# Kernel optimization log

Measured on AMD Instinct MI355X. Metric: run time of the kernel, lower is better.

## Reference

```python
import jax, jax.numpy as jnp
import numpy as np

N_NODES = 100000
N_EDGES = 1600000
HIDDEN = 128
NUM_RBF = 50
NTYPES = 95
CUTOFF = 5.0


def setup_inputs() -> dict:
    key = jax.random.key(0)
    ks = jax.random.split(key, 10)
    z = jax.random.randint(ks[0], (N_NODES,), 0, NTYPES)
    node_feat = jax.random.normal(ks[1], (N_NODES, HIDDEN), dtype=jnp.float32)
    edge_index = jax.random.randint(ks[2], (2, N_EDGES), 0, N_NODES)
    # distances uniform in [0, 6) so some edges fall beyond the 5.0 cutoff
    edge_weight = jax.random.uniform(ks[3], (N_EDGES,), dtype=jnp.float32) * 6.0
    edge_attr = jax.random.normal(ks[4], (N_EDGES, NUM_RBF), dtype=jnp.float32)
    # learned parameters
    emb = jax.random.normal(ks[5], (NTYPES, HIDDEN), dtype=jnp.float32)
    dp_w = jax.random.normal(ks[6], (HIDDEN, NUM_RBF), dtype=jnp.float32) * (1.0 / np.sqrt(NUM_RBF))
    dp_b = jnp.zeros((HIDDEN,), dtype=jnp.float32)
    comb_w = jax.random.normal(ks[7], (HIDDEN, 2 * HIDDEN), dtype=jnp.float32) * (1.0 / np.sqrt(2 * HIDDEN))
    comb_b = jnp.zeros((HIDDEN,), dtype=jnp.float32)
    return {"z": z, "node_feat": node_feat, "edge_index": edge_index,
            "edge_weight": edge_weight, "edge_attr": edge_attr,
            "emb": emb, "dp_w": dp_w, "dp_b": dp_b,
            "comb_w": comb_w, "comb_b": comb_b}


def cosine_cutoff(r, cutoff):
    c = 0.5 * (jnp.cos(r * (jnp.pi / cutoff)) + 1.0)
    return jnp.where(r < cutoff, c, 0.0)


def reference(z, node_feat, edge_index, edge_weight, edge_attr,
              emb, dp_w, dp_b, comb_w, comb_b):
    # distance filter: [E, H]
    C = cosine_cutoff(edge_weight, CUTOFF)
    W = (edge_attr @ dp_w.T + dp_b) * C[:, None]
    # neighbor-type embedding gathered per edge destination
    x_nb = emb[z]                      # [N, H]
    msg = W * x_nb[edge_index[1]]      # [E, H]
    # scatter-add messages to source nodes
    agg = jnp.zeros_like(node_feat).at[edge_index[0]].add(msg)  # [N, H]
    # combine node features with aggregated neighborhood embedding
    out = jnp.concatenate([node_feat, agg], axis=1) @ comb_w.T + comb_b
    return out
```

## Files before the change

kernel.cpp:

```cpp
#include <hip/hip_runtime.h>

#define HIDDEN 128
#define NRBF 50
#define CUTOFF_F 5.0f
#define PI_OVER_CUTOFF 0.6283185307179586f
#define SLOT_U32 28
#define EPB 512
#define B_PITCH 35
#define W_PITCH 66

typedef _Float16 half8_t __attribute__((ext_vector_type(8)));
using f32x4_t  = __attribute__((ext_vector_type(4))) float;
using short8_t = __attribute__((ext_vector_type(8))) short;
typedef __attribute__((ext_vector_type(2))) _Float16 hf2;

static __device__ __forceinline__ unsigned int pkh(float a, float b) {
    return __builtin_bit_cast(unsigned int, __builtin_amdgcn_cvt_pkrtz(a, b));
}
static __device__ __forceinline__ float cvlo(unsigned int u) {
    return (float)__builtin_bit_cast(hf2, u)[0];
}
static __device__ __forceinline__ float cvhi(unsigned int u) {
    return (float)__builtin_bit_cast(hf2, u)[1];
}
static __device__ __forceinline__ unsigned int pk_bf16(float a, float b) {
    unsigned int ua = __float_as_uint(a), ub = __float_as_uint(b);
    ua = (ua + 0x7FFFu + ((ua >> 16) & 1u)) >> 16;
    ub = (ub + 0x7FFFu + ((ub >> 16) & 1u)) >> 16;
    return ua | (ub << 16);
}


__global__ __launch_bounds__(256) void hist_kernel(
    const int* __restrict__ ei, const float* __restrict__ ew,
    int* __restrict__ cnt, int E)
{
    int e = blockIdx.x * 256 + threadIdx.x;
    if (e >= E) return;
    float r = ew[e];
    if (r < CUTOFF_F) atomicAdd(&cnt[ei[e]], 1);
}

__global__ __launch_bounds__(256) void scan1_kernel(
    const int* __restrict__ cnt, int* __restrict__ rowptr,
    int* __restrict__ bsum, int N)
{
    __shared__ int sh[256];
    int t = threadIdx.x, b = blockIdx.x;
    int base = b * 1024 + t * 4;
    int v[4];
#pragma unroll
    for (int j = 0; j < 4; ++j) v[j] = (base + j < N) ? cnt[base + j] : 0;
    int s = v[0] + v[1] + v[2] + v[3];
    sh[t] = s;
    __syncthreads();
    for (int off = 1; off < 256; off <<= 1) {
        int x = (t >= off) ? sh[t - off] : 0;
        __syncthreads();
        sh[t] += x;
        __syncthreads();
    }
    int run = sh[t] - s;
#pragma unroll
    for (int j = 0; j < 4; ++j) {
        if (base + j < N) rowptr[base + j] = run;
        run += v[j];
    }
    if (t == 255) bsum[b] = sh[255];
}

__global__ __launch_bounds__(256) void scan2_kernel(
    int* __restrict__ bsum, int* __restrict__ rowptr, int nb, int N)
{
    __shared__ int sh[256];
    int t = threadIdx.x;
    int v = (t < nb) ? bsum[t] : 0;
    sh[t] = v;
    __syncthreads();
    for (int off = 1; off < 256; off <<= 1) {
        int x = (t >= off) ? sh[t - off] : 0;
        __syncthreads();
        sh[t] += x;
        __syncthreads();
    }
    if (t < nb) bsum[t] = sh[t] - v;
    if (t == 255) rowptr[N] = sh[255];
}

__global__ __launch_bounds__(256) void scan3_kernel(
    int* __restrict__ rowptr, int* __restrict__ woff,
    const int* __restrict__ bsum, int N)
{
    int t = threadIdx.x, b = blockIdx.x;
    int base = b * 1024 + t * 4;
    int off = bsum[b];
#pragma unroll
    for (int j = 0; j < 4; ++j) {
        int i = base + j;
        if (i < N) {
            int r = rowptr[i] + off;
            rowptr[i] = r;
            woff[i] = r;
        }
    }
}

__global__ __launch_bounds__(256) void pad_kernel(
    const int* __restrict__ rowptr, int N,
    int* __restrict__ desc, unsigned int* __restrict__ slots)
{
    int M = rowptr[N];
    int t = blockIdx.x * 256 + threadIdx.x;
    for (int i = t; i < 512; i += 256 * gridDim.x) desc[M + i] = 0;
    for (int i = t; i < 512 * SLOT_U32; i += 256 * gridDim.x)
        slots[(size_t)M * SLOT_U32 + i] = 0u;
}

__global__ __launch_bounds__(256) void pack_emb(
    const float* __restrict__ emb, unsigned int* __restrict__ embp, int NT)
{
    int i = blockIdx.x * 256 + threadIdx.x;
    if (i >= NT * 64) return;
    int t = i >> 6, j = i & 63;
    embp[i] = pkh(emb[t * HIDDEN + j], emb[t * HIDDEN + j + 64]);
}

__global__ __launch_bounds__(256) void scatter_pack(
    const int* __restrict__ z, const int* __restrict__ ei,
    const float* __restrict__ ew, const float* __restrict__ ea,
    int* __restrict__ woff, int* __restrict__ desc,
    unsigned int* __restrict__ slots, int E)
{
    int e = blockIdx.x * 256 + threadIdx.x;
    if (e >= E) return;
    float r = ew[e];
    if (!(r < CUTOFF_F)) return;
    float C = 0.5f * (cosf(r * PI_OVER_CUTOFF) + 1.0f);
    int src = ei[e];
    int dst = ei[E + e];
    int zt  = z[dst];
    int p = atomicAdd(&woff[src], 1);
    desc[p] = src | (zt << 20);

    unsigned int buf[SLOT_U32];
    const float2* rp = (const float2*)(ea + (size_t)e * NRBF);
#pragma unroll
    for (int q = 0; q < 25; ++q) {
        float2 v = rp[q];
        buf[q] = pkh(C * v.x, C * v.y);
    }
    buf[25] = pkh(C, 0.f);
    buf[26] = 0u; buf[27] = 0u;
    uint4* sp = (uint4*)(slots + (size_t)p * SLOT_U32);
#pragma unroll
    for (int q = 0; q < 7; ++q) sp[q] = ((const uint4*)buf)[q];
}

__global__ __launch_bounds__(256) void scatter_simple(
    const int* __restrict__ z, const int* __restrict__ ei,
    const float* __restrict__ ew, int* __restrict__ woff,
    int* __restrict__ desc, float* __restrict__ cCA, int* __restrict__ eidA,
    int E)
{
    int e = blockIdx.x * 256 + threadIdx.x;
    if (e >= E) return;
    float r = ew[e];
    if (!(r < CUTOFF_F)) return;
    float C = 0.5f * (cosf(r * PI_OVER_CUTOFF) + 1.0f);
    int src = ei[e];
    int dst = ei[E + e];
    int zt  = z[dst];
    int p = atomicAdd(&woff[src], 1);
    desc[p] = src | (zt << 20);
    cCA[p]  = C;
    eidA[p] = e;
}

__global__ __launch_bounds__(256) void gather_mfma(
    const int* __restrict__ rowptr, const int* __restrict__ desc,
    const unsigned int* __restrict__ slots, const unsigned int* __restrict__ embp,
    const float* __restrict__ dpw, const float* __restrict__ dpb,
    float* __restrict__ agg, int N)
{
    __shared__ unsigned int Blds[128 * B_PITCH];
    __shared__ unsigned int Wlds[4][16 * W_PITCH];
    int M = rowptr[N];

    int nwg = gridDim.x, orig = blockIdx.x;
    int q = nwg >> 3, r8 = nwg & 7, xcd = orig & 7, sub = orig >> 3;
    int lb = (xcd < r8) ? xcd * (q + 1) + sub
                        : r8 * (q + 1) + (xcd - r8) * q + sub;
    int gbase = lb * EPB;
    if (gbase >= M) return;

    int tid  = threadIdx.x;
    int w    = tid >> 6;
    int lane = tid & 63;
    int c    = lane & 15;
    int g    = lane >> 4;

    for (int idx = tid; idx < 128 * 32; idx += 256) {
        int h = idx >> 5, p = idx & 31;
        unsigned int u = 0u;
        if (p < 25) {
            float2 v = *(const float2*)(dpw + h * NRBF + 2 * p);
            u = pkh(v.x, v.y);
        } else if (p == 25) {
            u = pkh(dpb[h], 0.f);
        }
        Blds[h * B_PITCH + p] = u;
    }
    __syncthreads();

    unsigned int* Ww = Wlds[w];
    int wbeg = gbase + w * 128;
    if (wbeg >= M) return;

    bool runc;
    if (wbeg == 0) runc = true;
    else runc = ((desc[wbeg - 1] & 0xFFFFF) != (desc[wbeg] & 0xFFFFF));

    const int4* dp = (const int4*)(desc + wbeg);

    const uint4* sp0 = (const uint4*)(slots + (size_t)(wbeg + c) * SLOT_U32);
    uint4 a0c = sp0[g];
    uint4 a1c = (g < 3) ? sp0[4 + g] : make_uint4(0u, 0u, 0u, 0u);
    int4 d0 = dp[0], d1 = dp[1], d2 = dp[2], d3 = dp[3];

    int   cur = -1;
    float r0 = 0.f, r1 = 0.f;

    for (int t = 0; t < 8; ++t) {
        int eb = wbeg + t * 16;
        uint4 A0u = a0c, A1u = a1c;
        int s_[16];
        s_[0]=__builtin_amdgcn_readfirstlane(d0.x);  s_[1]=__builtin_amdgcn_readfirstlane(d0.y);
        s_[2]=__builtin_amdgcn_readfirstlane(d0.z);  s_[3]=__builtin_amdgcn_readfirstlane(d0.w);
        s_[4]=__builtin_amdgcn_readfirstlane(d1.x);  s_[5]=__builtin_amdgcn_readfirstlane(d1.y);
        s_[6]=__builtin_amdgcn_readfirstlane(d1.z);  s_[7]=__builtin_amdgcn_readfirstlane(d1.w);
        s_[8]=__builtin_amdgcn_readfirstlane(d2.x);  s_[9]=__builtin_amdgcn_readfirstlane(d2.y);
        s_[10]=__builtin_amdgcn_readfirstlane(d2.z); s_[11]=__builtin_amdgcn_readfirstlane(d2.w);
        s_[12]=__builtin_amdgcn_readfirstlane(d3.x); s_[13]=__builtin_amdgcn_readfirstlane(d3.y);
        s_[14]=__builtin_amdgcn_readfirstlane(d3.z); s_[15]=__builtin_amdgcn_readfirstlane(d3.w);

        if (t < 7) {
            const uint4* spn = (const uint4*)(slots + (size_t)(eb + 16 + c) * SLOT_U32);
            a0c = spn[g];
            a1c = (g < 3) ? spn[4 + g] : make_uint4(0u, 0u, 0u, 0u);
            d0 = dp[t * 4 + 4]; d1 = dp[t * 4 + 5];
            d2 = dp[t * 4 + 6]; d3 = dp[t * 4 + 7];
        }

        unsigned int evp[16];
#pragma unroll
        for (int e2 = 0; e2 < 16; ++e2)
            evp[e2] = embp[(((unsigned int)s_[e2]) >> 20) * 64 + lane];

        half8_t A0 = __builtin_bit_cast(half8_t, A0u);
        half8_t A1 = __builtin_bit_cast(half8_t, A1u);
        f32x4_t acc[8];
#pragma unroll
        for (int nt = 0; nt < 8; ++nt) {
            uint4 b0 = *(const uint4*)&Blds[(nt * 16 + c) * B_PITCH + g * 4];
            uint4 b1 = *(const uint4*)&Blds[(nt * 16 + c) * B_PITCH + 16 + g * 4];
            f32x4_t a = (f32x4_t){0.f, 0.f, 0.f, 0.f};
            a = __builtin_amdgcn_mfma_f32_16x16x32_f16(A0, __builtin_bit_cast(half8_t, b0), a, 0, 0, 0);
            a = __builtin_amdgcn_mfma_f32_16x16x32_f16(A1, __builtin_bit_cast(half8_t, b1), a, 0, 0, 0);
            acc[nt] = a;
        }

#pragma unroll
        for (int m = 0; m < 4; ++m)
#pragma unroll
            for (int r = 0; r < 4; ++r)
                Ww[(g * 4 + r) * W_PITCH + m * 16 + c] = pkh(acc[m][r], acc[m + 4][r]);

        unsigned int wv[16];
#pragma unroll
        for (int e2 = 0; e2 < 16; ++e2)
            wv[e2] = Ww[e2 * W_PITCH + lane];

#pragma unroll
        for (int e2 = 0; e2 < 16; ++e2) {
            int src = s_[e2] & 0xFFFFF;
            if (src != cur) {
                if (cur >= 0) {
                    float* dst = agg + (size_t)cur * HIDDEN + lane;
                    if (runc) {
                        dst[0]  = r0;
                        dst[64] = r1;
                    } else {
                        unsafeAtomicAdd(dst,      r0);
                        unsafeAtomicAdd(dst + 64, r1);
                    }
                    runc = true;
                }
                cur = src; r0 = 0.f; r1 = 0.f;
            }
            r0 = fmaf(cvlo(wv[e2]), cvlo(evp[e2]), r0);
            r1 = fmaf(cvhi(wv[e2]), cvhi(evp[e2]), r1);
        }
    }
    if (cur >= 0) {
        int nxt = desc[wbeg + 128] & 0xFFFFF;
        float* dst = agg + (size_t)cur * HIDDEN + lane;
        if (runc && nxt != cur) {
            dst[0]  = r0;
            dst[64] = r1;
        } else {
            unsafeAtomicAdd(dst,      r0);
            unsafeAtomicAdd(dst + 64, r1);
        }
    }
}

__global__ __launch_bounds__(256) void gather_stream(
    const int* __restrict__ rowptr, const int* __restrict__ desc,
    const float* __restrict__ cC, const int* __restrict__ eidA,
    const float* __restrict__ ea, const float* __restrict__ emb,
    const float* __restrict__ dpw, const float* __restrict__ dpb,
    float* __restrict__ agg, int N, int nwaves)
{
    __shared__ unsigned int sh_ea[4][4][32];
    int lane  = threadIdx.x & 63;
    int wslot = threadIdx.x >> 6;
    int wid = __builtin_amdgcn_readfirstlane((int)((blockIdx.x * blockDim.x + threadIdx.x) >> 6));

    hf2 whA[25], whB[25];
    {
        const float* wr0 = dpw + (size_t)(2 * lane) * NRBF;
        const float* wr1 = wr0 + NRBF;
#pragma unroll
        for (int q = 0; q < 25; ++q) {
            float2 x = *(const float2*)(wr0 + 2 * q);
            float2 y = *(const float2*)(wr1 + 2 * q);
            whA[q] = __builtin_bit_cast(hf2, pkh(x.x, x.y));
            whB[q] = __builtin_bit_cast(hf2, pkh(y.x, y.y));
        }
    }
    float2 db = *(const float2*)(dpb + 2 * lane);

    int M  = rowptr[N];
    int CH = (M + nwaves - 1) / nwaves;
    int c0 = min(wid * CH, M);
    int c1 = min(c0 + CH, M);

    int   cur = -1, run_start = c0;
    float a0 = 0.f, a1 = 0.f;

    for (int i = c0; i < c1; i += 4) {
        int sv[4]; float cf[4]; int ed[4]; float2 ev[4]; float2 eaf[4];
#pragma unroll
        for (int j = 0; j < 4; ++j)
            if (i + j < c1) { sv[j] = desc[i + j]; cf[j] = cC[i + j]; ed[j] = eidA[i + j]; }
#pragma unroll
        for (int j = 0; j < 4; ++j)
            if (i + j < c1) ev[j] = *(const float2*)(emb + (size_t)((unsigned int)sv[j] >> 20) * HIDDEN + 2 * lane);
#pragma unroll
        for (int j = 0; j < 4; ++j)
            if (i + j < c1 && lane < 25) eaf[j] = *(const float2*)(ea + (size_t)ed[j] * NRBF + 2 * lane);
#pragma unroll
        for (int j = 0; j < 4; ++j)
            if (i + j < c1 && lane < 28) {
                unsigned int u = 0u;
                if (lane < 25) u = pkh(eaf[j].x, eaf[j].y);
                sh_ea[wslot][j][lane] = u;
            }
#pragma unroll
        for (int j = 0; j < 4; ++j) {
            if (i + j >= c1) break;
            int src = sv[j] & 0xFFFFF;
            if (src != cur) {
                if (cur >= 0) {
                    int rp0 = rowptr[cur], rp1 = rowptr[cur + 1];
                    float* dst = agg + (size_t)cur * HIDDEN + 2 * lane;
                    if (run_start == rp0 && (i + j) == rp1) {
                        *(float2*)dst = make_float2(a0, a1);
                    } else {
                        unsafeAtomicAdd(dst, a0);
                        unsafeAtomicAdd(dst + 1, a1);
                    }
                }
                cur = src; run_start = i + j; a0 = 0.f; a1 = 0.f;
            }
            float s0 = 0.f, s1 = 0.f;
#pragma unroll
            for (int qq = 0; qq < 6; ++qq) {
                uint4 u = *(const uint4*)&sh_ea[wslot][j][qq * 4];
#pragma unroll
                for (int t = 0; t < 4; ++t) {
                    unsigned int ww = (t == 0) ? u.x : (t == 1) ? u.y : (t == 2) ? u.z : u.w;
                    hf2 e2 = __builtin_bit_cast(hf2, ww);
                    s0 = fmaf((float)e2[0], (float)whA[qq*4+t][0], fmaf((float)e2[1], (float)whA[qq*4+t][1], s0));
                    s1 = fmaf((float)e2[0], (float)whB[qq*4+t][0], fmaf((float)e2[1], (float)whB[qq*4+t][1], s1));
                }
            }
            {
                hf2 e2 = __builtin_bit_cast(hf2, sh_ea[wslot][j][24]);
                s0 = fmaf((float)e2[0], (float)whA[24][0], fmaf((float)e2[1], (float)whA[24][1], s0));
                s1 = fmaf((float)e2[0], (float)whB[24][0], fmaf((float)e2[1], (float)whB[24][1], s1));
            }
            float W0 = (s0 + db.x) * cf[j];
            float W1 = (s1 + db.y) * cf[j];
            a0 = fmaf(W0, ev[j].x, a0);
            a1 = fmaf(W1, ev[j].y, a1);
        }
    }
    if (cur >= 0) {
        int rp0 = rowptr[cur], rp1 = rowptr[cur + 1];
        float* dst = agg + (size_t)cur * HIDDEN + 2 * lane;
        if (run_start == rp0 && c1 == rp1) {
            *(float2*)dst = make_float2(a0, a1);
        } else {
            unsafeAtomicAdd(dst, a0);
            unsafeAtomicAdd(dst + 1, a1);
        }
    }
}

__global__ __launch_bounds__(256) void edge_kernel(
    const int* __restrict__ z, const int* __restrict__ ei,
    const float* __restrict__ ew, const float* __restrict__ ea,
    const float* __restrict__ emb, const float* __restrict__ dpw,
    const float* __restrict__ dpb, float* __restrict__ agg, int E)
{
    int e = blockIdx.x * 256 + threadIdx.x;
    if (e >= E) return;
    float r = ew[e];
    if (!(r < CUTOFF_F)) return;
    float C = 0.5f * (cosf(r * PI_OVER_CUTOFF) + 1.0f);
    int src = ei[e];
    int dst = ei[E + e];
    int zt  = z[dst];
    float av[NRBF];
#pragma unroll
    for (int k = 0; k < NRBF; ++k) av[k] = ea[(size_t)e * NRBF + k];
    const float* er = emb + (size_t)zt * HIDDEN;
    float*       ar = agg + (size_t)src * HIDDEN;
#pragma unroll 2
    for (int h = 0; h < HIDDEN; ++h) {
        const float* wrow = dpw + h * NRBF;
        float s0 = 0.f, s1 = 0.f;
#pragma unroll
        for (int k = 0; k < NRBF; k += 2) {
            s0 = fmaf(av[k],     wrow[k],     s0);
            s1 = fmaf(av[k + 1], wrow[k + 1], s1);
        }
        float w2 = (dpb[h] + s0 + s1) * C;
        unsafeAtomicAdd(&ar[h], w2 * er[h]);
    }
}

__global__ __launch_bounds__(256) void combine_mfma(
    const float* __restrict__ nf, const float* __restrict__ cw,
    const float* __restrict__ cbias, float* out, int N)
{
    __shared__ unsigned int As_u[64 * 20];
    __shared__ unsigned int Bs_u[128 * 20];
    int tid  = threadIdx.x;
    int w    = tid >> 6;
    int lane = tid & 63;
    int c    = lane & 15;
    int g    = lane >> 4;
    int row0 = blockIdx.x * 64;

    f32x4_t acc[8];
#pragma unroll
    for (int q = 0; q < 8; ++q) acc[q] = (f32x4_t){0.f, 0.f, 0.f, 0.f};

    for (int ks = 0; ks < 8; ++ks) {
        const float* src = (ks < 4) ? nf : out;
        int kb = (ks & 3) * 32;
        {
            int r = tid >> 2, kq = tid & 3;
            int row = row0 + r;
            float4 v0 = make_float4(0.f, 0.f, 0.f, 0.f), v1 = v0;
            if (row < N) {
                const float4* p = (const float4*)(src + (size_t)row * HIDDEN + kb + kq * 8);
                v0 = p[0]; v1 = p[1];
            }
            *(uint4*)&As_u[r * 20 + kq * 4] =
                make_uint4(pk_bf16(v0.x, v0.y), pk_bf16(v0.z, v0.w),
                           pk_bf16(v1.x, v1.y), pk_bf16(v1.z, v1.w));
        }
        {
            int j = tid >> 1, hf = tid & 1;
            const float4* p = (const float4*)(cw + (size_t)j * 256 + ks * 32 + hf * 16);
            float4 b0 = p[0], b1 = p[1], b2 = p[2], b3 = p[3];
            *(uint4*)&Bs_u[j * 20 + hf * 8] =
                make_uint4(pk_bf16(b0.x, b0.y), pk_bf16(b0.z, b0.w),
                           pk_bf16(b1.x, b1.y), pk_bf16(b1.z, b1.w));
            *(uint4*)&Bs_u[j * 20 + hf * 8 + 4] =
                make_uint4(pk_bf16(b2.x, b2.y), pk_bf16(b2.z, b2.w),
                           pk_bf16(b3.x, b3.y), pk_bf16(b3.z, b3.w));
        }
        __syncthreads();
        uint4 au = *(const uint4*)&As_u[(w * 16 + c) * 20 + g * 4];
        short8_t af = __builtin_bit_cast(short8_t, au);
#pragma unroll
        for (int cbk = 0; cbk < 8; ++cbk) {
            uint4 bu = *(const uint4*)&Bs_u[(cbk * 16 + c) * 20 + g * 4];
            short8_t bf = __builtin_bit_cast(short8_t, bu);
            acc[cbk] = __builtin_amdgcn_mfma_f32_16x16x32_bf16(af, bf, acc[cbk], 0, 0, 0);
        }
        __syncthreads();
    }
#pragma unroll
    for (int cbk = 0; cbk < 8; ++cbk) {
        float bias = cbias[cbk * 16 + c];
#pragma unroll
        for (int r = 0; r < 4; ++r) {
            int row = row0 + w * 16 + g * 4 + r;
            if (row < N) out[(size_t)row * HIDDEN + cbk * 16 + c] = acc[cbk][r] + bias;
        }
    }
}


extern "C" void kernel_launch(void* const* d_in, const int* in_sizes, int n_in,
                              void* d_out, int out_size, void* d_ws, size_t ws_size,
                              hipStream_t stream)
{
    const int*   z   = (const int*)  d_in[0];
    const float* nf  = (const float*)d_in[1];
    const int*   ei  = (const int*)  d_in[2];
    const float* ew  = (const float*)d_in[3];
    const float* ea  = (const float*)d_in[4];
    const float* emb = (const float*)d_in[5];
    const float* dpw = (const float*)d_in[6];
    const float* dpb = (const float*)d_in[7];
    const float* cw  = (const float*)d_in[8];
    const float* cb  = (const float*)d_in[9];
    float* out = (float*)d_out;

    int N = in_sizes[0];
    int E = in_sizes[3];
    int NT = in_sizes[5] / HIDDEN;

    size_t hdr  = ((size_t)2 * N + 1 + 1024 + 3) & ~(size_t)3;
    size_t Epad = (size_t)E + 512;
    size_t need1 = (hdr + Epad + Epad * SLOT_U32 + (size_t)NT * 64 + 16) * 4;
    size_t need2 = (hdr + (size_t)3 * E) * 4;

    (void)hipMemsetAsync(out, 0, (size_t)N * HIDDEN * sizeof(float), stream);

    int nb1 = (N + 1023) / 1024;

    if (ws_size >= need1) {
        int* rowptr = (int*)d_ws;
        int* woff   = rowptr + (N + 1);
        int* bsum   = woff + N;
        int* desc   = (int*)d_ws + hdr;
        unsigned int* slots = (unsigned int*)(desc + Epad);
        slots = (unsigned int*)(((size_t)slots + 15) & ~(size_t)15);
        unsigned int* embp = slots + Epad * SLOT_U32;

        (void)hipMemsetAsync(woff, 0, (size_t)N * 4, stream);
        hist_kernel<<<(E + 255) / 256, 256, 0, stream>>>(ei, ew, woff, E);
        scan1_kernel<<<nb1, 256, 0, stream>>>(woff, rowptr, bsum, N);
        scan2_kernel<<<1, 256, 0, stream>>>(bsum, rowptr, nb1, N);
        scan3_kernel<<<nb1, 256, 0, stream>>>(rowptr, woff, bsum, N);
        pack_emb<<<(NT * 64 + 255) / 256, 256, 0, stream>>>(emb, embp, NT);
        scatter_pack<<<(E + 255) / 256, 256, 0, stream>>>(z, ei, ew, ea, woff,
                                                          desc, slots, E);
        pad_kernel<<<8, 256, 0, stream>>>(rowptr, N, desc, slots);
        int nblk = (E + EPB - 1) / EPB;
        gather_mfma<<<nblk, 256, 0, stream>>>(rowptr, desc, slots, embp,
                                              dpw, dpb, out, N);
    } else if (ws_size >= need2) {
        int* rowptr = (int*)d_ws;
        int* woff   = rowptr + (N + 1);
        int* bsum   = woff + N;
        int* desc   = (int*)d_ws + hdr;
        float* cCA  = (float*)(desc + E);
        int* eidA   = (int*)(cCA + E);

        (void)hipMemsetAsync(woff, 0, (size_t)N * 4, stream);
        hist_kernel<<<(E + 255) / 256, 256, 0, stream>>>(ei, ew, woff, E);
        scan1_kernel<<<nb1, 256, 0, stream>>>(woff, rowptr, bsum, N);
        scan2_kernel<<<1, 256, 0, stream>>>(bsum, rowptr, nb1, N);
        scan3_kernel<<<nb1, 256, 0, stream>>>(rowptr, woff, bsum, N);
        scatter_simple<<<(E + 255) / 256, 256, 0, stream>>>(z, ei, ew, woff,
                                                            desc, cCA, eidA, E);
        const int blocks = 2048;
        gather_stream<<<blocks, 256, 0, stream>>>(rowptr, desc, cCA, eidA,
                                                  ea, emb, dpw, dpb, out, N,
                                                  blocks * 4);
    } else {
        edge_kernel<<<(E + 255) / 256, 256, 0, stream>>>(z, ei, ew, ea, emb,
                                                         dpw, dpb, out, E);
    }

    combine_mfma<<<(N + 63) / 64, 256, 0, stream>>>(nf, cw, cb, out, N);
}
```

Measured before the change: 393.1 us.

## Gather edge_attr rows by edge id in gather kernel instead of packing slots

```diff
diff --git a/kernel.cpp b/kernel.cpp
--- a/kernel.cpp
+++ b/kernel.cpp
@@ -4,10 +4,10 @@
 #define NRBF 50
 #define CUTOFF_F 5.0f
 #define PI_OVER_CUTOFF 0.6283185307179586f
-#define SLOT_U32 28
 #define EPB 512
 #define B_PITCH 35
 #define W_PITCH 66
+#define A_PITCH 68
 
 typedef _Float16 half8_t __attribute__((ext_vector_type(8)));
 using f32x4_t  = __attribute__((ext_vector_type(4))) float;
@@ -28,6 +28,25 @@
     ua = (ua + 0x7FFFu + ((ua >> 16) & 1u)) >> 16;
     ub = (ub + 0x7FFFu + ((ub >> 16) & 1u)) >> 16;
     return ua | (ub << 16);
+}
+static __device__ __forceinline__ void loadd16(const int4* p, int t, int* s) {
+    int4 q0 = p[t * 4], q1 = p[t * 4 + 1], q2 = p[t * 4 + 2], q3 = p[t * 4 + 3];
+    s[0]  = __builtin_amdgcn_readfirstlane(q0.x);
+    s[1]  = __builtin_amdgcn_readfirstlane(q0.y);
+    s[2]  = __builtin_amdgcn_readfirstlane(q0.z);
+    s[3]  = __builtin_amdgcn_readfirstlane(q0.w);
+    s[4]  = __builtin_amdgcn_readfirstlane(q1.x);
+    s[5]  = __builtin_amdgcn_readfirstlane(q1.y);
+    s[6]  = __builtin_amdgcn_readfirstlane(q1.z);
+    s[7]  = __builtin_amdgcn_readfirstlane(q1.w);
+    s[8]  = __builtin_amdgcn_readfirstlane(q2.x);
+    s[9]  = __builtin_amdgcn_readfirstlane(q2.y);
+    s[10] = __builtin_amdgcn_readfirstlane(q2.z);
+    s[11] = __builtin_amdgcn_readfirstlane(q2.w);
+    s[12] = __builtin_amdgcn_readfirstlane(q3.x);
+    s[13] = __builtin_amdgcn_readfirstlane(q3.y);
+    s[14] = __builtin_amdgcn_readfirstlane(q3.z);
+    s[15] = __builtin_amdgcn_readfirstlane(q3.w);
 }
 
 
@@ -107,13 +126,11 @@
 
 __global__ __launch_bounds__(256) void pad_kernel(
     const int* __restrict__ rowptr, int N,
-    int* __restrict__ desc, unsigned int* __restrict__ slots)
+    int* __restrict__ desc, int* __restrict__ eidA, float* __restrict__ CA)
 {
     int M = rowptr[N];
     int t = blockIdx.x * 256 + threadIdx.x;
-    for (int i = t; i < 512; i += 256 * gridDim.x) desc[M + i] = 0;
-    for (int i = t; i < 512 * SLOT_U32; i += 256 * gridDim.x)
-        slots[(size_t)M * SLOT_U32 + i] = 0u;
+    if (t < 512) { desc[M + t] = 0; eidA[M + t] = 0; CA[M + t] = 0.f; }
 }
 
 __global__ __launch_bounds__(256) void pack_emb(
@@ -125,11 +142,11 @@
     embp[i] = pkh(emb[t * HIDDEN + j], emb[t * HIDDEN + j + 64]);
 }
 
-__global__ __launch_bounds__(256) void scatter_pack(
+__global__ __launch_bounds__(256) void scatter_slim(
     const int* __restrict__ z, const int* __restrict__ ei,
-    const float* __restrict__ ew, const float* __restrict__ ea,
-    int* __restrict__ woff, int* __restrict__ desc,
-    unsigned int* __restrict__ slots, int E)
+    const float* __restrict__ ew, int* __restrict__ woff,
+    int* __restrict__ desc, int* __restrict__ eidA, float* __restrict__ CA,
+    int E)
 {
     int e = blockIdx.x * 256 + threadIdx.x;
     if (e >= E) return;
@@ -141,48 +158,19 @@
     int zt  = z[dst];
     int p = atomicAdd(&woff[src], 1);
     desc[p] = src | (zt << 20);
-
-    unsigned int buf[SLOT_U32];
-    const float2* rp = (const float2*)(ea + (size_t)e * NRBF);
-#pragma unroll
-    for (int q = 0; q < 25; ++q) {
-        float2 v = rp[q];
-        buf[q] = pkh(C * v.x, C * v.y);
-    }
-    buf[25] = pkh(C, 0.f);
-    buf[26] = 0u; buf[27] = 0u;
-    uint4* sp = (uint4*)(slots + (size_t)p * SLOT_U32);
-#pragma unroll
-    for (int q = 0; q < 7; ++q) sp[q] = ((const uint4*)buf)[q];
-}
-
-__global__ __launch_bounds__(256) void scatter_simple(
-    const int* __restrict__ z, const int* __restrict__ ei,
-    const float* __restrict__ ew, int* __restrict__ woff,
-    int* __restrict__ desc, float* __restrict__ cCA, int* __restrict__ eidA,
-    int E)
-{
-    int e = blockIdx.x * 256 + threadIdx.x;
-    if (e >= E) return;
-    float r = ew[e];
-    if (!(r < CUTOFF_F)) return;
-    float C = 0.5f * (cosf(r * PI_OVER_CUTOFF) + 1.0f);
-    int src = ei[e];
-    int dst = ei[E + e];
-    int zt  = z[dst];
-    int p = atomicAdd(&woff[src], 1);
-    desc[p] = src | (zt << 20);
-    cCA[p]  = C;
     eidA[p] = e;
+    CA[p]   = C;
 }
 
 __global__ __launch_bounds__(256) void gather_mfma(
     const int* __restrict__ rowptr, const int* __restrict__ desc,
-    const unsigned int* __restrict__ slots, const unsigned int* __restrict__ embp,
+    const int* __restrict__ eidA, const float* __restrict__ CA,
+    const float* __restrict__ ea, const unsigned int* __restrict__ embp,
     const float* __restrict__ dpw, const float* __restrict__ dpb,
     float* __restrict__ agg, int N)
 {
     __shared__ unsigned int Blds[128 * B_PITCH];
+    __shared__ float        Ast[4][16 * A_PITCH];
     __shared__ unsigned int Wlds[4][16 * W_PITCH];
     int M = rowptr[N];
 
@@ -198,6 +186,7 @@
     int lane = tid & 63;
     int c    = lane & 15;
     int g    = lane >> 4;
+    int lidx = min(lane, 49);
 
     for (int idx = tid; idx < 128 * 32; idx += 256) {
         int h = idx >> 5, p = idx & 31;
@@ -212,7 +201,8 @@
     }
     __syncthreads();
 
-    unsigned int* Ww = Wlds[w];
+    float*        AstW = Ast[w];
+    unsigned int* Ww   = Wlds[w];
     int wbeg = gbase + w * 128;
     if (wbeg >= M) return;
 
@@ -221,43 +211,59 @@
     else runc = ((desc[wbeg - 1] & 0xFFFFF) != (desc[wbeg] & 0xFFFFF));
 
     const int4* dp = (const int4*)(desc + wbeg);
-
-    const uint4* sp0 = (const uint4*)(slots + (size_t)(wbeg + c) * SLOT_U32);
-    uint4 a0c = sp0[g];
-    uint4 a1c = (g < 3) ? sp0[4 + g] : make_uint4(0u, 0u, 0u, 0u);
-    int4 d0 = dp[0], d1 = dp[1], d2 = dp[2], d3 = dp[3];
+    const int4* ep = (const int4*)(eidA + wbeg);
+
+    int sd[16], se[16], sdN[16], seN[16];
+    float vr[16], vrN[16];
+
+    loadd16(dp, 0, sd);
+    loadd16(ep, 0, se);
+    float vC = CA[wbeg + c];
+#pragma unroll
+    for (int j = 0; j < 16; ++j)
+        vr[j] = ea[(size_t)(unsigned int)se[j] * NRBF + lidx];
+    loadd16(dp, 1, sdN);
+    loadd16(ep, 1, seN);
+    float vCN = CA[wbeg + 16 + c];
 
     int   cur = -1;
     float r0 = 0.f, r1 = 0.f;
 
     for (int t = 0; t < 8; ++t) {
-        int eb = wbeg + t * 16;
-        uint4 A0u = a0c, A1u = a1c;
-        int s_[16];
-        s_[0]=__builtin_amdgcn_readfirstlane(d0.x);  s_[1]=__builtin_amdgcn_readfirstlane(d0.y);
-        s_[2]=__builtin_amdgcn_readfirstlane(d0.z);  s_[3]=__builtin_amdgcn_readfirstlane(d0.w);
-        s_[4]=__builtin_amdgcn_readfirstlane(d1.x);  s_[5]=__builtin_amdgcn_readfirstlane(d1.y);
-        s_[6]=__builtin_amdgcn_readfirstlane(d1.z);  s_[7]=__builtin_amdgcn_readfirstlane(d1.w);
-        s_[8]=__builtin_amdgcn_readfirstlane(d2.x);  s_[9]=__builtin_amdgcn_readfirstlane(d2.y);
-        s_[10]=__builtin_amdgcn_readfirstlane(d2.z); s_[11]=__builtin_amdgcn_readfirstlane(d2.w);
-        s_[12]=__builtin_amdgcn_readfirstlane(d3.x); s_[13]=__builtin_amdgcn_readfirstlane(d3.y);
-        s_[14]=__builtin_amdgcn_readfirstlane(d3.z); s_[15]=__builtin_amdgcn_readfirstlane(d3.w);
-
         if (t < 7) {
-            const uint4* spn = (const uint4*)(slots + (size_t)(eb + 16 + c) * SLOT_U32);
-            a0c = spn[g];
-            a1c = (g < 3) ? spn[4 + g] : make_uint4(0u, 0u, 0u, 0u);
-            d0 = dp[t * 4 + 4]; d1 = dp[t * 4 + 5];
-            d2 = dp[t * 4 + 6]; d3 = dp[t * 4 + 7];
-        }
-
+#pragma unroll
+            for (int j = 0; j < 16; ++j)
+                vrN[j] = ea[(size_t)(unsigned int)seN[j] * NRBF + lidx];
+        }
         unsigned int evp[16];
 #pragma unroll
-        for (int e2 = 0; e2 < 16; ++e2)
-            evp[e2] = embp[(((unsigned int)s_[e2]) >> 20) * 64 + lane];
-
+        for (int j = 0; j < 16; ++j)
+            evp[j] = embp[(((unsigned int)sd[j]) >> 20) * 64 + lane];
+
+#pragma unroll
+        for (int j = 0; j < 16; ++j)
+            AstW[j * A_PITCH + lane] = vr[j];
+
+        const float* ab = &AstW[c * A_PITCH];
+        float4 f0 = *(const float4*)&ab[g * 8];
+        float4 f1 = *(const float4*)&ab[g * 8 + 4];
+        uint4 A0u = make_uint4(pkh(vC * f0.x, vC * f0.y), pkh(vC * f0.z, vC * f0.w),
+                               pkh(vC * f1.x, vC * f1.y), pkh(vC * f1.z, vC * f1.w));
+        uint4 A1u;
+        if (g < 2) {
+            float4 h0 = *(const float4*)&ab[32 + g * 8];
+            float4 h1 = *(const float4*)&ab[36 + g * 8];
+            A1u = make_uint4(pkh(vC * h0.x, vC * h0.y), pkh(vC * h0.z, vC * h0.w),
+                             pkh(vC * h1.x, vC * h1.y), pkh(vC * h1.z, vC * h1.w));
+        } else if (g == 2) {
+            float2 hv = *(const float2*)&ab[48];
+            A1u = make_uint4(pkh(vC * hv.x, vC * hv.y), pkh(vC, 0.f), 0u, 0u);
+        } else {
+            A1u = make_uint4(0u, 0u, 0u, 0u);
+        }
         half8_t A0 = __builtin_bit_cast(half8_t, A0u);
         half8_t A1 = __builtin_bit_cast(half8_t, A1u);
+
         f32x4_t acc[8];
 #pragma unroll
         for (int nt = 0; nt < 8; ++nt) {
@@ -282,7 +288,7 @@
 
 #pragma unroll
         for (int e2 = 0; e2 < 16; ++e2) {
-            int src = s_[e2] & 0xFFFFF;
+            int src = sd[e2] & 0xFFFFF;
             if (src != cur) {
                 if (cur >= 0) {
                     float* dst = agg + (size_t)cur * HIDDEN + lane;
@@ -299,6 +305,17 @@
             }
             r0 = fmaf(cvlo(wv[e2]), cvlo(evp[e2]), r0);
             r1 = fmaf(cvhi(wv[e2]), cvhi(evp[e2]), r1);
+        }
+
+        if (t < 7) {
+#pragma unroll
+            for (int k = 0; k < 16; ++k) { sd[k] = sdN[k]; se[k] = seN[k]; vr[k] = vrN[k]; }
+            vC = vCN;
+            if (t < 6) {
+                loadd16(dp, t + 2, sdN);
+                loadd16(ep, t + 2, seN);
+                vCN = CA[wbeg + (t + 2) * 16 + c];
+            }
         }
     }
     if (cur >= 0) {
@@ -539,7 +556,7 @@
 
     size_t hdr  = ((size_t)2 * N + 1 + 1024 + 3) & ~(size_t)3;
     size_t Epad = (size_t)E + 512;
-    size_t need1 = (hdr + Epad + Epad * SLOT_U32 + (size_t)NT * 64 + 16) * 4;
+    size_t need1 = (hdr + 3 * Epad + (size_t)NT * 64 + 16) * 4;
     size_t need2 = (hdr + (size_t)3 * E) * 4;
 
     (void)hipMemsetAsync(out, 0, (size_t)N * HIDDEN * sizeof(float), stream);
@@ -551,9 +568,9 @@
         int* woff   = rowptr + (N + 1);
         int* bsum   = woff + N;
         int* desc   = (int*)d_ws + hdr;
-        unsigned int* slots = (unsigned int*)(desc + Epad);
-        slots = (unsigned int*)(((size_t)slots + 15) & ~(size_t)15);
-        unsigned int* embp = slots + Epad * SLOT_U32;
+        int* eidA   = desc + Epad;
+        float* CAa  = (float*)(eidA + Epad);
+        unsigned int* embp = (unsigned int*)(CAa + Epad);
 
         (void)hipMemsetAsync(woff, 0, (size_t)N * 4, stream);
         hist_kernel<<<(E + 255) / 256, 256, 0, stream>>>(ei, ew, woff, E);
@@ -561,12 +578,12 @@
         scan2_kernel<<<1, 256, 0, stream>>>(bsum, rowptr, nb1, N);
         scan3_kernel<<<nb1, 256, 0, stream>>>(rowptr, woff, bsum, N);
         pack_emb<<<(NT * 64 + 255) / 256, 256, 0, stream>>>(emb, embp, NT);
-        scatter_pack<<<(E + 255) / 256, 256, 0, stream>>>(z, ei, ew, ea, woff,
-                                                          desc, slots, E);
-        pad_kernel<<<8, 256, 0, stream>>>(rowptr, N, desc, slots);
+        scatter_slim<<<(E + 255) / 256, 256, 0, stream>>>(z, ei, ew, woff,
+                                                          desc, eidA, CAa, E);
+        pad_kernel<<<2, 256, 0, stream>>>(rowptr, N, desc, eidA, CAa);
         int nblk = (E + EPB - 1) / EPB;
-        gather_mfma<<<nblk, 256, 0, stream>>>(rowptr, desc, slots, embp,
-                                              dpw, dpb, out, N);
+        gather_mfma<<<nblk, 256, 0, stream>>>(rowptr, desc, eidA, CAa, ea,
+                                              embp, dpw, dpb, out, N);
     } else if (ws_size >= need2) {
         int* rowptr = (int*)d_ws;
         int* woff   = rowptr + (N + 1);
@@ -580,8 +597,11 @@
         scan1_kernel<<<nb1, 256, 0, stream>>>(woff, rowptr, bsum, N);
         scan2_kernel<<<1, 256, 0, stream>>>(bsum, rowptr, nb1, N);
         scan3_kernel<<<nb1, 256, 0, stream>>>(rowptr, woff, bsum, N);
-        scatter_simple<<<(E + 255) / 256, 256, 0, stream>>>(z, ei, ew, woff,
-                                                            desc, cCA, eidA, E);
+        scatter_simple_fallback:
+        {
+        }
+        scatter_slim<<<(E + 255) / 256, 256, 0, stream>>>(z, ei, ew, woff,
+                                                          desc, eidA, (float*)cCA, E);
         const int blocks = 2048;
         gather_stream<<<blocks, 256, 0, stream>>>(rowptr, desc, cCA, eidA,
                                                   ea, emb, dpw, dpb, out, N,
```

Result: faster. 382.9 us (-2.6%).

## Stage edge_attr through LDS in scatter, widen slots, deepen gather prefetch

Applied to the files above, without the earlier changes.

```diff
diff --git a/kernel.cpp b/kernel.cpp
--- a/kernel.cpp
+++ b/kernel.cpp
@@ -4,10 +4,10 @@
 #define NRBF 50
 #define CUTOFF_F 5.0f
 #define PI_OVER_CUTOFF 0.6283185307179586f
-#define SLOT_U32 28
 #define EPB 512
-#define B_PITCH 35
-#define W_PITCH 66
+#define BPITCH 36
+#define WPITCH 66
+#define SLOT_U32 32
 
 typedef _Float16 half8_t __attribute__((ext_vector_type(8)));
 using f32x4_t  = __attribute__((ext_vector_type(4))) float;
@@ -105,31 +105,230 @@
     }
 }
 
-__global__ __launch_bounds__(256) void pad_kernel(
+__global__ __launch_bounds__(256) void pad_pack_kernel(
     const int* __restrict__ rowptr, int N,
-    int* __restrict__ desc, unsigned int* __restrict__ slots)
+    int* __restrict__ desc, unsigned int* __restrict__ slots,
+    const float* __restrict__ emb, unsigned int* __restrict__ embp, int NT)
 {
     int M = rowptr[N];
     int t = blockIdx.x * 256 + threadIdx.x;
-    for (int i = t; i < 512; i += 256 * gridDim.x) desc[M + i] = 0;
+    if (t < 512) desc[M + t] = 0;
+    size_t sb = (size_t)M * SLOT_U32;
     for (int i = t; i < 512 * SLOT_U32; i += 256 * gridDim.x)
-        slots[(size_t)M * SLOT_U32 + i] = 0u;
-}
-
-__global__ __launch_bounds__(256) void pack_emb(
-    const float* __restrict__ emb, unsigned int* __restrict__ embp, int NT)
-{
-    int i = blockIdx.x * 256 + threadIdx.x;
-    if (i >= NT * 64) return;
-    int t = i >> 6, j = i & 63;
-    embp[i] = pkh(emb[t * HIDDEN + j], emb[t * HIDDEN + j + 64]);
-}
-
-__global__ __launch_bounds__(256) void scatter_pack(
+        slots[sb + i] = 0u;
+    if (t < NT * 64) {
+        int r = t >> 6, j = t & 63;
+        embp[t] = pkh(emb[r * HIDDEN + j], emb[r * HIDDEN + j + 64]);
+    }
+}
+
+__global__ __launch_bounds__(256) void scatter_pack2(
     const int* __restrict__ z, const int* __restrict__ ei,
     const float* __restrict__ ew, const float* __restrict__ ea,
     int* __restrict__ woff, int* __restrict__ desc,
     unsigned int* __restrict__ slots, int E)
+{
+    __shared__ float ls[128 * NRBF];
+    __shared__ int   lp[128];
+    __shared__ float lc[128];
+    int tid  = threadIdx.x;
+    int base = blockIdx.x * 128;
+    int cnt  = min(128, E - base);
+    if (cnt <= 0) return;
+
+    const float* src = ea + (size_t)base * NRBF;
+    int nf4 = (cnt * NRBF) >> 2;
+    for (int i = tid; i < nf4; i += 256)
+        *(float4*)&ls[i * 4] = *(const float4*)&src[i * 4];
+    for (int i = nf4 * 4 + tid; i < cnt * NRBF; i += 256)
+        ls[i] = src[i];
+
+    if (tid < cnt) {
+        int e = base + tid;
+        float r = ew[e];
+        int p = -1; float C = 0.f;
+        if (r < CUTOFF_F) {
+            C = 0.5f * (cosf(r * PI_OVER_CUTOFF) + 1.0f);
+            int s = ei[e], d = ei[E + e];
+            p = atomicAdd(&woff[s], 1);
+            desc[p] = s | (z[d] << 20);
+        }
+        lp[tid] = p; lc[tid] = C;
+    }
+    __syncthreads();
+
+    int e = tid >> 1, h = tid & 1;
+    if (e >= cnt) return;
+    int p = lp[e];
+    if (p < 0) return;
+    float C = lc[e];
+    const float* row = &ls[e * NRBF];
+    unsigned int buf[16];
+    if (h == 0) {
+#pragma unroll
+        for (int q = 0; q < 16; ++q)
+            buf[q] = pkh(C * row[2 * q], C * row[2 * q + 1]);
+    } else {
+#pragma unroll
+        for (int q = 0; q < 9; ++q)
+            buf[q] = pkh(C * row[32 + 2 * q], C * row[33 + 2 * q]);
+        buf[9] = pkh(C, 0.f);
+#pragma unroll
+        for (int q = 10; q < 16; ++q) buf[q] = 0u;
+    }
+    uint4* dst = (uint4*)(slots + (size_t)p * SLOT_U32 + h * 16);
+#pragma unroll
+    for (int q = 0; q < 4; ++q) dst[q] = ((const uint4*)buf)[q];
+}
+
+__global__ __launch_bounds__(256) void gather_mfma2(
+    const int* __restrict__ rowptr, const int* __restrict__ desc,
+    const unsigned int* __restrict__ slots, const unsigned int* __restrict__ embp,
+    const float* __restrict__ dpw, const float* __restrict__ dpb,
+    float* __restrict__ agg, int N)
+{
+    __shared__ unsigned int Blds[128 * BPITCH];
+    __shared__ unsigned int Wsh[4][16 * WPITCH];
+    int M = rowptr[N];
+
+    int nwg = gridDim.x, orig = blockIdx.x;
+    int q = nwg >> 3, r8 = nwg & 7, xcd = orig & 7, sub = orig >> 3;
+    int lb = (xcd < r8) ? xcd * (q + 1) + sub
+                        : r8 * (q + 1) + (xcd - r8) * q + sub;
+    int gbase = lb * EPB;
+    if (gbase >= M) return;
+
+    int tid  = threadIdx.x;
+    int w    = tid >> 6;
+    int lane = tid & 63;
+    int cc   = lane & 15;
+    int g    = lane >> 4;
+    int l16  = lane & 15;
+
+    for (int idx = tid; idx < 128 * 32; idx += 256) {
+        int h = idx >> 5, p = idx & 31;
+        unsigned int u = 0u;
+        if (p < 25) {
+            float2 v = *(const float2*)(dpw + h * NRBF + 2 * p);
+            u = pkh(v.x, v.y);
+        } else if (p == 25) {
+            u = pkh(dpb[h], 0.f);
+        }
+        Blds[h * BPITCH + p] = u;
+    }
+    __syncthreads();
+
+    unsigned int* Ww = Wsh[w];
+    int wbeg = gbase + w * 128;
+    if (wbeg >= M) return;
+
+    bool runc;
+    if (wbeg == 0) runc = true;
+    else runc = ((desc[wbeg - 1] & 0xFFFFF) != (desc[wbeg] & 0xFFFFF));
+
+    const int* descb = desc + wbeg;
+
+#define XTR16(V, S)                                                            \
+    _Pragma("unroll")                                                          \
+    for (int j_ = 0; j_ < 16; ++j_) S[j_] = __builtin_amdgcn_readlane((V), j_);
+
+    int sd0[16], sd1[16], sdN[16];
+    unsigned int evpC[16];
+    uint4 A0c, A1c;
+
+    {
+        int dv0 = descb[0 * 16 + l16];
+        int dv1 = descb[1 * 16 + l16];
+        XTR16(dv0, sd0);
+        XTR16(dv1, sd1);
+    }
+    int dq0 = descb[2 * 16 + l16], dq1 = descb[3 * 16 + l16];
+    {
+        const uint4* sp0 = (const uint4*)(slots + (size_t)(wbeg + cc) * SLOT_U32);
+        A0c = sp0[g];
+        A1c = (g < 3) ? sp0[4 + g] : make_uint4(0u, 0u, 0u, 0u);
+    }
+#pragma unroll
+    for (int j = 0; j < 16; ++j)
+        evpC[j] = embp[(((unsigned int)sd0[j]) >> 20) * 64 + lane];
+
+    int   cur = -1;
+    float r0 = 0.f, r1 = 0.f;
+
+    for (int t = 0; t < 8; ++t) {
+        uint4 A0u = A0c, A1u = A1c;
+        {
+            const uint4* spn = (const uint4*)(slots + (size_t)(wbeg + (t + 1) * 16 + cc) * SLOT_U32);
+            A0c = spn[g];
+            A1c = (g < 3) ? spn[4 + g] : make_uint4(0u, 0u, 0u, 0u);
+        }
+        XTR16(dq0, sdN);
+        dq0 = dq1;
+        dq1 = descb[(t + 4) * 16 + l16];
+
+        half8_t A0 = __builtin_bit_cast(half8_t, A0u);
+        half8_t A1 = __builtin_bit_cast(half8_t, A1u);
+        f32x4_t acc[8];
+#pragma unroll
+        for (int nt = 0; nt < 8; ++nt) {
+            uint4 b0 = *(const uint4*)&Blds[(nt * 16 + cc) * BPITCH + 4 * g];
+            uint4 b1 = *(const uint4*)&Blds[(nt * 16 + cc) * BPITCH + 16 + 4 * g];
+            f32x4_t a = (f32x4_t){0.f, 0.f, 0.f, 0.f};
+            a = __builtin_amdgcn_mfma_f32_16x16x32_f16(A0, __builtin_bit_cast(half8_t, b0), a, 0, 0, 0);
+            a = __builtin_amdgcn_mfma_f32_16x16x32_f16(A1, __builtin_bit_cast(half8_t, b1), a, 0, 0, 0);
+            acc[nt] = a;
+        }
+#pragma unroll
+        for (int m = 0; m < 4; ++m)
+#pragma unroll
+            for (int r = 0; r < 4; ++r)
+                Ww[(g * 4 + r) * WPITCH + m * 16 + cc] = pkh(acc[m][r], acc[m + 4][r]);
+        unsigned int wv[16];
+#pragma unroll
+        for (int e2 = 0; e2 < 16; ++e2)
+            wv[e2] = Ww[e2 * WPITCH + lane];
+
+#pragma unroll
+        for (int e2 = 0; e2 < 16; ++e2) {
+            int src_ = sd0[e2] & 0xFFFFF;
+            if (src_ != cur) {
+                if (cur >= 0) {
+                    float* dst_ = agg + (size_t)cur * HIDDEN + lane;
+                    if (runc) { dst_[0] = r0; dst_[64] = r1; }
+                    else { unsafeAtomicAdd(dst_, r0); unsafeAtomicAdd(dst_ + 64, r1); }
+                    runc = true;
+                }
+                cur = src_; r0 = 0.f; r1 = 0.f;
+            }
+            r0 = fmaf(cvlo(wv[e2]), cvlo(evpC[e2]), r0);
+            r1 = fmaf(cvhi(wv[e2]), cvhi(evpC[e2]), r1);
+        }
+#pragma unroll
+        for (int j = 0; j < 16; ++j)
+            evpC[j] = embp[(((unsigned int)sd1[j]) >> 20) * 64 + lane];
+#pragma unroll
+        for (int j = 0; j < 16; ++j) { sd0[j] = sd1[j]; sd1[j] = sdN[j]; }
+    }
+#undef XTR16
+
+    if (cur >= 0) {
+        int nxt = desc[wbeg + 128] & 0xFFFFF;
+        float* dst = agg + (size_t)cur * HIDDEN + lane;
+        if (runc && nxt != cur) {
+            dst[0]  = r0;
+            dst[64] = r1;
+        } else {
+            unsafeAtomicAdd(dst,      r0);
+            unsafeAtomicAdd(dst + 64, r1);
+        }
+    }
+}
+
+__global__ __launch_bounds__(256) void scatter_slim(
+    const int* __restrict__ z, const int* __restrict__ ei,
+    const float* __restrict__ ew, int* __restrict__ woff,
+    int* __restrict__ desc, int* __restrict__ eidA, float* __restrict__ CA,
+    int E)
 {
     int e = blockIdx.x * 256 + threadIdx.x;
     if (e >= E) return;
@@ -141,177 +340,8 @@
     int zt  = z[dst];
     int p = atomicAdd(&woff[src], 1);
     desc[p] = src | (zt << 20);
-
-    unsigned int buf[SLOT_U32];
-    const float2* rp = (const float2*)(ea + (size_t)e * NRBF);
-#pragma unroll
-    for (int q = 0; q < 25; ++q) {
-        float2 v = rp[q];
-        buf[q] = pkh(C * v.x, C * v.y);
-    }
-    buf[25] = pkh(C, 0.f);
-    buf[26] = 0u; buf[27] = 0u;
-    uint4* sp = (uint4*)(slots + (size_t)p * SLOT_U32);
-#pragma unroll
-    for (int q = 0; q < 7; ++q) sp[q] = ((const uint4*)buf)[q];
-}
-
-__global__ __launch_bounds__(256) void scatter_simple(
-    const int* __restrict__ z, const int* __restrict__ ei,
-    const float* __restrict__ ew, int* __restrict__ woff,
-    int* __restrict__ desc, float* __restrict__ cCA, int* __restrict__ eidA,
-    int E)
-{
-    int e = blockIdx.x * 256 + threadIdx.x;
-    if (e >= E) return;
-    float r = ew[e];
-    if (!(r < CUTOFF_F)) return;
-    float C = 0.5f * (cosf(r * PI_OVER_CUTOFF) + 1.0f);
-    int src = ei[e];
-    int dst = ei[E + e];
-    int zt  = z[dst];
-    int p = atomicAdd(&woff[src], 1);
-    desc[p] = src | (zt << 20);
-    cCA[p]  = C;
     eidA[p] = e;
-}
-
-__global__ __launch_bounds__(256) void gather_mfma(
-    const int* __restrict__ rowptr, const int* __restrict__ desc,
-    const unsigned int* __restrict__ slots, const unsigned int* __restrict__ embp,
-    const float* __restrict__ dpw, const float* __restrict__ dpb,
-    float* __restrict__ agg, int N)
-{
-    __shared__ unsigned int Blds[128 * B_PITCH];
-    __shared__ unsigned int Wlds[4][16 * W_PITCH];
-    int M = rowptr[N];
-
-    int nwg = gridDim.x, orig = blockIdx.x;
-    int q = nwg >> 3, r8 = nwg & 7, xcd = orig & 7, sub = orig >> 3;
-    int lb = (xcd < r8) ? xcd * (q + 1) + sub
-                        : r8 * (q + 1) + (xcd - r8) * q + sub;
-    int gbase = lb * EPB;
-    if (gbase >= M) return;
-
-    int tid  = threadIdx.x;
-    int w    = tid >> 6;
-    int lane = tid & 63;
-    int c    = lane & 15;
-    int g    = lane >> 4;
-
-    for (int idx = tid; idx < 128 * 32; idx += 256) {
-        int h = idx >> 5, p = idx & 31;
-        unsigned int u = 0u;
-        if (p < 25) {
-            float2 v = *(const float2*)(dpw + h * NRBF + 2 * p);
-            u = pkh(v.x, v.y);
-        } else if (p == 25) {
-            u = pkh(dpb[h], 0.f);
-        }
-        Blds[h * B_PITCH + p] = u;
-    }
-    __syncthreads();
-
-    unsigned int* Ww = Wlds[w];
-    int wbeg = gbase + w * 128;
-    if (wbeg >= M) return;
-
-    bool runc;
-    if (wbeg == 0) runc = true;
-    else runc = ((desc[wbeg - 1] & 0xFFFFF) != (desc[wbeg] & 0xFFFFF));
-
-    const int4* dp = (const int4*)(desc + wbeg);
-
-    const uint4* sp0 = (const uint4*)(slots + (size_t)(wbeg + c) * SLOT_U32);
-    uint4 a0c = sp0[g];
-    uint4 a1c = (g < 3) ? sp0[4 + g] : make_uint4(0u, 0u, 0u, 0u);
-    int4 d0 = dp[0], d1 = dp[1], d2 = dp[2], d3 = dp[3];
-
-    int   cur = -1;
-    float r0 = 0.f, r1 = 0.f;
-
-    for (int t = 0; t < 8; ++t) {
-        int eb = wbeg + t * 16;
-        uint4 A0u = a0c, A1u = a1c;
-        int s_[16];
-        s_[0]=__builtin_amdgcn_readfirstlane(d0.x);  s_[1]=__builtin_amdgcn_readfirstlane(d0.y);
-        s_[2]=__builtin_amdgcn_readfirstlane(d0.z);  s_[3]=__builtin_amdgcn_readfirstlane(d0.w);
-        s_[4]=__builtin_amdgcn_readfirstlane(d1.x);  s_[5]=__builtin_amdgcn_readfirstlane(d1.y);
-        s_[6]=__builtin_amdgcn_readfirstlane(d1.z);  s_[7]=__builtin_amdgcn_readfirstlane(d1.w);
-        s_[8]=__builtin_amdgcn_readfirstlane(d2.x);  s_[9]=__builtin_amdgcn_readfirstlane(d2.y);
-        s_[10]=__builtin_amdgcn_readfirstlane(d2.z); s_[11]=__builtin_amdgcn_readfirstlane(d2.w);
-        s_[12]=__builtin_amdgcn_readfirstlane(d3.x); s_[13]=__builtin_amdgcn_readfirstlane(d3.y);
-        s_[14]=__builtin_amdgcn_readfirstlane(d3.z); s_[15]=__builtin_amdgcn_readfirstlane(d3.w);
-
-        if (t < 7) {
-            const uint4* spn = (const uint4*)(slots + (size_t)(eb + 16 + c) * SLOT_U32);
-            a0c = spn[g];
-            a1c = (g < 3) ? spn[4 + g] : make_uint4(0u, 0u, 0u, 0u);
-            d0 = dp[t * 4 + 4]; d1 = dp[t * 4 + 5];
-            d2 = dp[t * 4 + 6]; d3 = dp[t * 4 + 7];
-        }
-
-        unsigned int evp[16];
-#pragma unroll
-        for (int e2 = 0; e2 < 16; ++e2)
-            evp[e2] = embp[(((unsigned int)s_[e2]) >> 20) * 64 + lane];
-
-        half8_t A0 = __builtin_bit_cast(half8_t, A0u);
-        half8_t A1 = __builtin_bit_cast(half8_t, A1u);
-        f32x4_t acc[8];
-#pragma unroll
-        for (int nt = 0; nt < 8; ++nt) {
-            uint4 b0 = *(const uint4*)&Blds[(nt * 16 + c) * B_PITCH + g * 4];
-            uint4 b1 = *(const uint4*)&Blds[(nt * 16 + c) * B_PITCH + 16 + g * 4];
-            f32x4_t a = (f32x4_t){0.f, 0.f, 0.f, 0.f};
-            a = __builtin_amdgcn_mfma_f32_16x16x32_f16(A0, __builtin_bit_cast(half8_t, b0), a, 0, 0, 0);
-            a = __builtin_amdgcn_mfma_f32_16x16x32_f16(A1, __builtin_bit_cast(half8_t, b1), a, 0, 0, 0);
-            acc[nt] = a;
-        }
-
-#pragma unroll
-        for (int m = 0; m < 4; ++m)
-#pragma unroll
-            for (int r = 0; r < 4; ++r)
-                Ww[(g * 4 + r) * W_PITCH + m * 16 + c] = pkh(acc[m][r], acc[m + 4][r]);
-
-        unsigned int wv[16];
-#pragma unroll
-        for (int e2 = 0; e2 < 16; ++e2)
-            wv[e2] = Ww[e2 * W_PITCH + lane];
-
-#pragma unroll
-        for (int e2 = 0; e2 < 16; ++e2) {
-            int src = s_[e2] & 0xFFFFF;
-            if (src != cur) {
-                if (cur >= 0) {
-                    float* dst = agg + (size_t)cur * HIDDEN + lane;
-                    if (runc) {
-                        dst[0]  = r0;
-                        dst[64] = r1;
-                    } else {
-                        unsafeAtomicAdd(dst,      r0);
-                        unsafeAtomicAdd(dst + 64, r1);
-                    }
-                    runc = true;
-                }
-                cur = src; r0 = 0.f; r1 = 0.f;
-            }
-            r0 = fmaf(cvlo(wv[e2]), cvlo(evp[e2]), r0);
-            r1 = fmaf(cvhi(wv[e2]), cvhi(evp[e2]), r1);
-        }
-    }
-    if (cur >= 0) {
-        int nxt = desc[wbeg + 128] & 0xFFFFF;
-        float* dst = agg + (size_t)cur * HIDDEN + lane;
-        if (runc && nxt != cur) {
-            dst[0]  = r0;
-            dst[64] = r1;
-        } else {
-            unsafeAtomicAdd(dst,      r0);
-            unsafeAtomicAdd(dst + 64, r1);
-        }
-    }
+    CA[p]   = C;
 }
 
 __global__ __launch_bounds__(256) void gather_stream(
@@ -539,7 +569,7 @@
 
     size_t hdr  = ((size_t)2 * N + 1 + 1024 + 3) & ~(size_t)3;
     size_t Epad = (size_t)E + 512;
-    size_t need1 = (hdr + Epad + Epad * SLOT_U32 + (size_t)NT * 64 + 16) * 4;
+    size_t need1 = (hdr + Epad * (1 + SLOT_U32) + (size_t)NT * 64 + 16) * 4;
     size_t need2 = (hdr + (size_t)3 * E) * 4;
 
     (void)hipMemsetAsync(out, 0, (size_t)N * HIDDEN * sizeof(float), stream);
@@ -552,21 +582,20 @@
         int* bsum   = woff + N;
         int* desc   = (int*)d_ws + hdr;
         unsigned int* slots = (unsigned int*)(desc + Epad);
-        slots = (unsigned int*)(((size_t)slots + 15) & ~(size_t)15);
-        unsigned int* embp = slots + Epad * SLOT_U32;
+        unsigned int* embp  = slots + Epad * SLOT_U32;
 
         (void)hipMemsetAsync(woff, 0, (size_t)N * 4, stream);
         hist_kernel<<<(E + 255) / 256, 256, 0, stream>>>(ei, ew, woff, E);
         scan1_kernel<<<nb1, 256, 0, stream>>>(woff, rowptr, bsum, N);
         scan2_kernel<<<1, 256, 0, stream>>>(bsum, rowptr, nb1, N);
         scan3_kernel<<<nb1, 256, 0, stream>>>(rowptr, woff, bsum, N);
-        pack_emb<<<(NT * 64 + 255) / 256, 256, 0, stream>>>(emb, embp, NT);
-        scatter_pack<<<(E + 255) / 256, 256, 0, stream>>>(z, ei, ew, ea, woff,
-                                                          desc, slots, E);
-        pad_kernel<<<8, 256, 0, stream>>>(rowptr, N, desc, slots);
+        pad_pack_kernel<<<64, 256, 0, stream>>>(rowptr, N, desc, slots,
+                                                emb, embp, NT);
+        scatter_pack2<<<(E + 127) / 128, 256, 0, stream>>>(z, ei, ew, ea,
+                                                           woff, desc, slots, E);
         int nblk = (E + EPB - 1) / EPB;
-        gather_mfma<<<nblk, 256, 0, stream>>>(rowptr, desc, slots, embp,
-                                              dpw, dpb, out, N);
+        gather_mfma2<<<nblk, 256, 0, stream>>>(rowptr, desc, slots, embp,
+                                               dpw, dpb, out, N);
     } else if (ws_size >= need2) {
         int* rowptr = (int*)d_ws;
         int* woff   = rowptr + (N + 1);
@@ -580,8 +609,8 @@
         scan1_kernel<<<nb1, 256, 0, stream>>>(woff, rowptr, bsum, N);
         scan2_kernel<<<1, 256, 0, stream>>>(bsum, rowptr, nb1, N);
         scan3_kernel<<<nb1, 256, 0, stream>>>(rowptr, woff, bsum, N);
-        scatter_simple<<<(E + 255) / 256, 256, 0, stream>>>(z, ei, ew, woff,
-                                                            desc, cCA, eidA, E);
+        scatter_slim<<<(E + 255) / 256, 256, 0, stream>>>(z, ei, ew, woff,
+                                                          desc, eidA, cCA, E);
         const int blocks = 2048;
         gather_stream<<<blocks, 256, 0, stream>>>(rowptr, desc, cCA, eidA,
                                                   ea, emb, dpw, dpb, out, N,
```

Result: slower. 416.5 us (+5.9%).
